# Kernel optimization log

Measured on AMD Instinct MI355X. Metric: run time of the kernel, lower is better.

## Reference

```python
import jax, jax.numpy as jnp
import numpy as np

V, E, H, L, T, B = 6500, 192, 6, 6, 512, 32
HS = E // H  # 32
EPS = 1e-5


def setup_inputs() -> dict:
    key = jax.random.key(0)
    ks = jax.random.split(key, 9)
    s = 0.02
    return {
        "idx": jax.random.randint(ks[0], (B, T), 0, V, dtype=jnp.int32),
        "tok_emb": jax.random.normal(ks[1], (V, E), dtype=jnp.float32) * s,
        "Wq": jax.random.normal(ks[2], (L, E, E), dtype=jnp.float32) * s,
        "Wk": jax.random.normal(ks[3], (L, E, E), dtype=jnp.float32) * s,
        "Wv": jax.random.normal(ks[4], (L, E, E), dtype=jnp.float32) * s,
        "Wo": jax.random.normal(ks[5], (L, E, E), dtype=jnp.float32) * s,
        "W1": jax.random.normal(ks[6], (L, E, 4 * E), dtype=jnp.float32) * s,
        "W2": jax.random.normal(ks[7], (L, 4 * E, E), dtype=jnp.float32) * s,
        "ln1_g": jnp.ones((L, E)), "ln1_b": jnp.zeros((L, E)),
        "ln2_g": jnp.ones((L, E)), "ln2_b": jnp.zeros((L, E)),
        "lnf_g": jnp.ones((E,)), "lnf_b": jnp.zeros((E,)),
        "Wlm": jax.random.normal(ks[8], (E, V), dtype=jnp.float32) * s,
    }


def _layer_norm(x, g, b):
    mu = jnp.mean(x, axis=-1, keepdims=True)
    var = jnp.mean(jnp.square(x - mu), axis=-1, keepdims=True)
    return (x - mu) * jax.lax.rsqrt(var + EPS) * g + b


def _sinusoidal(t, d):
    pos = jnp.arange(t, dtype=jnp.float32)[:, None]
    div = jnp.exp(jnp.arange(0, d, 2, dtype=jnp.float32) * (-np.log(10000.0) / d))
    pe = jnp.zeros((t, d), dtype=jnp.float32)
    pe = pe.at[:, 0::2].set(jnp.sin(pos * div))
    pe = pe.at[:, 1::2].set(jnp.cos(pos * div))
    return pe


def reference(idx, tok_emb, Wq, Wk, Wv, Wo, W1, W2,
              ln1_g, ln1_b, ln2_g, ln2_b, lnf_g, lnf_b, Wlm):
    x = tok_emb[idx] + _sinusoidal(T, E)[None, :, :]  # [B,T,E]
    mask = jnp.tril(jnp.ones((T, T), dtype=bool))
    scale = E ** (-0.5)  # NOTE: original scales by n_embd**-0.5, not head_size

    def block(x, p):
        l1g, l1b, wq, wk, wv, wo, l2g, l2b, w1, w2 = p
        h = _layer_norm(x, l1g, l1b)
        q = jnp.einsum('bte,ehd->bhtd', h, wq.reshape(E, H, HS))
        k = jnp.einsum('bte,ehd->bhtd', h, wk.reshape(E, H, HS))
        v = jnp.einsum('bte,ehd->bhtd', h, wv.reshape(E, H, HS))
        wei = jnp.einsum('bhtd,bhsd->bhts', q, k) * scale  # [B,H,T,T]
        wei = jnp.where(mask, wei, -jnp.inf)
        wei = jax.nn.softmax(wei, axis=-1)
        att = jnp.einsum('bhts,bhsd->bthd', wei, v).reshape(B, T, E)
        x = x + att @ wo
        h2 = _layer_norm(x, l2g, l2b)
        x = x + jax.nn.gelu(h2 @ w1, approximate=False) @ w2
        return x, None

    x, _ = jax.lax.scan(block, x, (ln1_g, ln1_b, Wq, Wk, Wv, Wo, ln2_g, ln2_b, W1, W2))
    x = _layer_norm(x, lnf_g, lnf_b)
    return x @ Wlm  # [B,T,V] logits
```

## Files before the change

### kernel.cpp

```cpp
#include <hip/hip_runtime.h>
#include <hip/hip_bf16.h>
#include <math.h>

#define VOCAB 6500
#define EMB   192
#define NH    6
#define NL    6
#define SEQ   512
#define BATCH 32
#define HSZ   32
#define BT    (BATCH*SEQ)

typedef __attribute__((ext_vector_type(8))) short bh8;
typedef __attribute__((ext_vector_type(4))) float f32x4;

#define ATT_SCALE 0.07216878364870323f

__global__ __launch_bounds__(256) void embed_ln(
    const int* __restrict__ idx, const float* __restrict__ tok,
    const float* __restrict__ g, const float* __restrict__ b,
    float* __restrict__ x, __hip_bfloat16* __restrict__ h) {
  const int wid = threadIdx.x >> 6, lane = threadIdx.x & 63;
  const int bt = blockIdx.x * 4 + wid;
  const int t  = bt & (SEQ - 1);
  const int tokid = idx[bt];
  float v[3];
  #pragma unroll
  for (int i = 0; i < 3; ++i) {
    const int e = lane + i * 64;
    const int i2 = e & ~1;
    const float div = expf((float)i2 * (-9.210340371976184f / (float)EMB));
    const float ang = (float)t * div;
    const float pe  = (e & 1) ? cosf(ang) : sinf(ang);
    v[i] = tok[(size_t)tokid * EMB + e] + pe;
  }
  float s = v[0] + v[1] + v[2];
  #pragma unroll
  for (int o = 32; o; o >>= 1) s += __shfl_xor(s, o);
  const float mu = s * (1.0f / (float)EMB);
  float vs = 0.f;
  #pragma unroll
  for (int i = 0; i < 3; ++i) { const float d = v[i] - mu; vs += d * d; }
  #pragma unroll
  for (int o = 32; o; o >>= 1) vs += __shfl_xor(vs, o);
  const float r = rsqrtf(vs * (1.0f / (float)EMB) + 1e-5f);
  float* xr = x + (size_t)bt * EMB;
  __hip_bfloat16* hr = h + (size_t)bt * EMB;
  #pragma unroll
  for (int i = 0; i < 3; ++i) {
    const int e = lane + i * 64;
    xr[e] = v[i];
    hr[e] = __float2bfloat16((v[i] - mu) * r * g[e] + b[e]);
  }
}

__global__ __launch_bounds__(256) void wprep(
    const float* __restrict__ Wq, const float* __restrict__ Wk,
    const float* __restrict__ Wv, const float* __restrict__ Wo,
    const float* __restrict__ W1, const float* __restrict__ W2,
    const float* __restrict__ Wlm,
    __hip_bfloat16* __restrict__ wqkv, __hip_bfloat16* __restrict__ wot,
    __hip_bfloat16* __restrict__ w1t,  __hip_bfloat16* __restrict__ w2t,
    __hip_bfloat16* __restrict__ wlt) {
  __shared__ float t[32][33];
  const int id = blockIdx.x;
  const float* Ws; __hip_bfloat16* Wd; int K, N, bx, by;
  if (id < 864) {
    const int z = id / 36, rem = id % 36;
    const int sel = z / NL, layer = z % NL;
    by = rem / 6; bx = rem % 6; K = 192; N = 192;
    const float* s4[4] = {Wq, Wk, Wv, Wo};
    Ws = s4[sel] + (size_t)layer * 192 * 192;
    Wd = (sel < 3) ? wqkv + ((size_t)layer * 576 + sel * 192) * 192
                   : wot  + (size_t)layer * 192 * 192;
  } else if (id < 1728) {
    const int j = id - 864, layer = j / 144, rem = j % 144;
    bx = rem % 24; by = rem / 24; K = 192; N = 768;
    Ws = W1 + (size_t)layer * 192 * 768;
    Wd = w1t + (size_t)layer * 768 * 192;
  } else if (id < 2592) {
    const int j = id - 1728, layer = j / 144, rem = j % 144;
    bx = rem % 6; by = rem / 6; K = 768; N = 192;
    Ws = W2 + (size_t)layer * 768 * 192;
    Wd = w2t + (size_t)layer * 192 * 768;
  } else {
    const int j = id - 2592;
    bx = j % 204; by = j / 204; K = 192; N = VOCAB;
    Ws = Wlm; Wd = wlt;
  }
  const int kt = by * 32, nt = bx * 32;
  const int tx = threadIdx.x & 31, ty = threadIdx.x >> 5;
  for (int i = ty; i < 32; i += 8) {
    const int k = kt + i, n = nt + tx;
    t[i][tx] = (k < K && n < N) ? Ws[(size_t)k * N + n] : 0.f;
  }
  __syncthreads();
  for (int i = ty; i < 32; i += 8) {
    const int n = nt + i, k = kt + tx;
    if (n < N && k < K) Wd[(size_t)n * K + k] = __float2bfloat16(t[tx][i]);
  }
}

template<int EPI, int BN>
__global__ __launch_bounds__(256) void gemm_big(
    const __hip_bfloat16* __restrict__ A, const __hip_bfloat16* __restrict__ Bt,
    void* __restrict__ Cv, int M, int N, int K) {
  constexpr int LDK = 72;
  constexpr int NB = BN / 32;
  constexpr int NC = BN / 16;
  __shared__ short As[128 * LDK];
  __shared__ short Bs[BN * LDK];
  const int tid = threadIdx.x;
  const int wid = tid >> 6, lane = tid & 63;
  const int m0 = blockIdx.y * 128, n0 = blockIdx.x * BN;
  const int srow = tid >> 3, schk = tid & 7;
  const int fr = lane & 15, fg = lane >> 4;

  f32x4 acc[2][NC];
  #pragma unroll
  for (int rt = 0; rt < 2; ++rt)
    #pragma unroll
    for (int ct = 0; ct < NC; ++ct) acc[rt][ct] = (f32x4){0.f, 0.f, 0.f, 0.f};

  bh8 av[4], bv[NB];
  #pragma unroll
  for (int p = 0; p < 4; ++p)
    av[p] = *reinterpret_cast<const bh8*>(A + (size_t)(m0 + srow + p * 32) * K + schk * 8);
  #pragma unroll
  for (int p = 0; p < NB; ++p) {
    const int nr = n0 + srow + p * 32;
    if (nr < N) bv[p] = *reinterpret_cast<const bh8*>(Bt + (size_t)nr * K + schk * 8);
    else        bv[p] = (bh8){0,0,0,0,0,0,0,0};
  }

  for (int k0 = 0; k0 < K; k0 += 64) {
    __syncthreads();
    #pragma unroll
    for (int p = 0; p < 4; ++p)
      *reinterpret_cast<bh8*>(As + (srow + p * 32) * LDK + schk * 8) = av[p];
    #pragma unroll
    for (int p = 0; p < NB; ++p)
      *reinterpret_cast<bh8*>(Bs + (srow + p * 32) * LDK + schk * 8) = bv[p];
    __syncthreads();
    if (k0 + 64 < K) {
      const int kn = k0 + 64 + schk * 8;
      #pragma unroll
      for (int p = 0; p < 4; ++p)
        av[p] = *reinterpret_cast<const bh8*>(A + (size_t)(m0 + srow + p * 32) * K + kn);
      #pragma unroll
      for (int p = 0; p < NB; ++p) {
        const int nr = n0 + srow + p * 32;
        if (nr < N) bv[p] = *reinterpret_cast<const bh8*>(Bt + (size_t)nr * K + kn);
      }
    }
    #pragma unroll
    for (int s = 0; s < 2; ++s) {
      bh8 af[2];
      #pragma unroll
      for (int rt = 0; rt < 2; ++rt)
        af[rt] = *reinterpret_cast<const bh8*>(As + (wid * 32 + rt * 16 + fr) * LDK + s * 32 + fg * 8);
      #pragma unroll
      for (int ct = 0; ct < NC; ++ct) {
        const bh8 bf_ = *reinterpret_cast<const bh8*>(Bs + (ct * 16 + fr) * LDK + s * 32 + fg * 8);
        #pragma unroll
        for (int rt = 0; rt < 2; ++rt)
          acc[rt][ct] = __builtin_amdgcn_mfma_f32_16x16x32_bf16(af[rt], bf_, acc[rt][ct], 0, 0, 0);
      }
    }
  }

  #pragma unroll
  for (int rt = 0; rt < 2; ++rt)
    #pragma unroll
    for (int ct = 0; ct < NC; ++ct) {
      const int col = n0 + ct * 16 + fr;
      if (col < N) {
        #pragma unroll
        for (int rr = 0; rr < 4; ++rr) {
          const int row = m0 + wid * 32 + rt * 16 + fg * 4 + rr;
          float v = acc[rt][ct][rr];
          if (EPI == 0) {
            ((float*)Cv)[(size_t)row * N + col] = v;
          } else if (EPI == 2) {
            v = 0.5f * v * (1.0f + erff(v * 0.70710678118654752f));
            ((__hip_bfloat16*)Cv)[(size_t)row * N + col] = __float2bfloat16(v);
          } else {
            const int part = col / 192, c2 = col - part * 192;
            if (part == 0) v *= ATT_SCALE;
            const int bb = row >> 9, tt = row & (SEQ - 1);
            const int hh = c2 >> 5, dd = c2 & (HSZ - 1);
            ((__hip_bfloat16*)Cv)[(size_t)part * BT * EMB +
                (((size_t)(bb * NH + hh)) * SEQ + tt) * HSZ + dd] = __float2bfloat16(v);
          }
        }
      }
    }
}

__global__ __launch_bounds__(128) void gemm_resln(
    const __hip_bfloat16* __restrict__ A, const __hip_bfloat16* __restrict__ Bt,
    float* __restrict__ X, __hip_bfloat16* __restrict__ Hout,
    const float* __restrict__ g, const float* __restrict__ b, int K) {
  constexpr int LDK = 72;
  __shared__ short As[32 * LDK];
  __shared__ short Bs[192 * LDK];
  const int tid = threadIdx.x;
  const int wid = tid >> 6, lane = tid & 63;
  const int m0 = blockIdx.x * 32;
  const int srow = tid >> 3, schk = tid & 7;
  const int fr = lane & 15, fg = lane >> 4;

  f32x4 acc[12];
  #pragma unroll
  for (int j = 0; j < 12; ++j) acc[j] = (f32x4){0.f, 0.f, 0.f, 0.f};

  bh8 av[2], bv[12];
  #pragma unroll
  for (int p = 0; p < 2; ++p)
    av[p] = *reinterpret_cast<const bh8*>(A + (size_t)(m0 + srow + p * 16) * K + schk * 8);
  #pragma unroll
  for (int p = 0; p < 12; ++p)
    bv[p] = *reinterpret_cast<const bh8*>(Bt + (size_t)(srow + p * 16) * K + schk * 8);

  for (int k0 = 0; k0 < K; k0 += 64) {
    __syncthreads();
    #pragma unroll
    for (int p = 0; p < 2; ++p)
      *reinterpret_cast<bh8*>(As + (srow + p * 16) * LDK + schk * 8) = av[p];
    #pragma unroll
    for (int p = 0; p < 12; ++p)
      *reinterpret_cast<bh8*>(Bs + (srow + p * 16) * LDK + schk * 8) = bv[p];
    __syncthreads();
    if (k0 + 64 < K) {
      const int kn = k0 + 64 + schk * 8;
      #pragma unroll
      for (int p = 0; p < 2; ++p)
        av[p] = *reinterpret_cast<const bh8*>(A + (size_t)(m0 + srow + p * 16) * K + kn);
      #pragma unroll
      for (int p = 0; p < 12; ++p)
        bv[p] = *reinterpret_cast<const bh8*>(Bt + (size_t)(srow + p * 16) * K + kn);
    }
    #pragma unroll
    for (int s = 0; s < 2; ++s) {
      const bh8 af = *reinterpret_cast<const bh8*>(As + (wid * 16 + fr) * LDK + s * 32 + fg * 8);
      #pragma unroll
      for (int j = 0; j < 12; ++j) {
        const bh8 bf_ = *reinterpret_cast<const bh8*>(Bs + (j * 16 + fr) * LDK + s * 32 + fg * 8);
        acc[j] = __builtin_amdgcn_mfma_f32_16x16x32_bf16(af, bf_, acc[j], 0, 0, 0);
      }
    }
  }

  #pragma unroll
  for (int rr = 0; rr < 4; ++rr) {
    const int row = m0 + wid * 16 + fg * 4 + rr;
    float v[12], sum = 0.f, sq = 0.f;
    #pragma unroll
    for (int j = 0; j < 12; ++j) {
      v[j] = acc[j][rr] + X[(size_t)row * EMB + j * 16 + fr];
      sum += v[j]; sq += v[j] * v[j];
    }
    #pragma unroll
    for (int o = 8; o; o >>= 1) {
      sum += __shfl_xor(sum, o);
      sq  += __shfl_xor(sq,  o);
    }
    const float mu = sum * (1.0f / (float)EMB);
    const float r  = rsqrtf(sq * (1.0f / (float)EMB) - mu * mu + 1e-5f);
    #pragma unroll
    for (int j = 0; j < 12; ++j) {
      const int col = j * 16 + fr;
      X[(size_t)row * EMB + col] = v[j];
      Hout[(size_t)row * EMB + col] = __float2bfloat16((v[j] - mu) * r * g[col] + b[col]);
    }
  }
}

__global__ __launch_bounds__(256) void flash_attn(
    const __hip_bfloat16* __restrict__ qh, const __hip_bfloat16* __restrict__ kh,
    const __hip_bfloat16* __restrict__ vh, __hip_bfloat16* __restrict__ att) {
  constexpr int QT = 128, KT = 128;
  constexpr int LK = 40;
  constexpr int LS = 136;
  __shared__ __hip_bfloat16 Ks[KT * LK];
  __shared__ __hip_bfloat16 Vs[HSZ * LS];
  __shared__ __hip_bfloat16 Ps[4][32 * LS];
  const int qt = (SEQ / QT - 1) - blockIdx.x;
  const int h = blockIdx.y, b = blockIdx.z;
  const int tid = threadIdx.x, wid = tid >> 6, lane = tid & 63;
  const int q0 = qt * QT;
  const size_t hb = ((size_t)(b * NH + h)) * SEQ * HSZ;
  const int fr = lane & 15, fg = lane >> 4;

  bh8 aq[2];
  #pragma unroll
  for (int rt = 0; rt < 2; ++rt)
    aq[rt] = *reinterpret_cast<const bh8*>(
        qh + hb + (size_t)(q0 + wid * 32 + rt * 16 + fr) * HSZ + fg * 8);

  f32x4 o[2][2];
  float lp[2][4];
  #pragma unroll
  for (int rt = 0; rt < 2; ++rt) {
    #pragma unroll
    for (int ct = 0; ct < 2; ++ct) o[rt][ct] = (f32x4){0.f, 0.f, 0.f, 0.f};
    #pragma unroll
    for (int rr = 0; rr < 4; ++rr) lp[rt][rr] = 0.f;
  }

  const int nt = qt + 1;
  const int sr = tid >> 1;
  const int dbase = (tid & 1) * 16;
  bh8 kv[2], vv[2];
  #pragma unroll
  for (int i = 0; i < 2; ++i) {
    kv[i] = *reinterpret_cast<const bh8*>(kh + hb + (size_t)sr * HSZ + dbase + i * 8);
    vv[i] = *reinterpret_cast<const bh8*>(vh + hb + (size_t)sr * HSZ + dbase + i * 8);
  }

  for (int it = 0; it < nt; ++it) {
    const int s0 = it * KT;
    __syncthreads();
    #pragma unroll
    for (int i = 0; i < 2; ++i) {
      const int d0 = dbase + i * 8;
      *reinterpret_cast<bh8*>(&Ks[sr * LK + d0]) = kv[i];
      short tmp[8]; *reinterpret_cast<bh8*>(tmp) = vv[i];
      #pragma unroll
      for (int j = 0; j < 8; ++j)
        Vs[(d0 + j) * LS + sr] = *reinterpret_cast<__hip_bfloat16*>(&tmp[j]);
    }
    __syncthreads();
    if (it + 1 < nt) {
      const size_t nb_ = hb + (size_t)(s0 + KT + sr) * HSZ + dbase;
      #pragma unroll
      for (int i = 0; i < 2; ++i) {
        kv[i] = *reinterpret_cast<const bh8*>(kh + nb_ + i * 8);
        vv[i] = *reinterpret_cast<const bh8*>(vh + nb_ + i * 8);
      }
    }

    f32x4 sfr[2][8];
    #pragma unroll
    for (int rt = 0; rt < 2; ++rt)
      #pragma unroll
      for (int st = 0; st < 8; ++st) {
        const bh8 bf_ = *reinterpret_cast<const bh8*>(&Ks[(st * 16 + fr) * LK + fg * 8]);
        sfr[rt][st] = __builtin_amdgcn_mfma_f32_16x16x32_bf16(
            aq[rt], bf_, (f32x4){0.f, 0.f, 0.f, 0.f}, 0, 0, 0);
      }

    __hip_bfloat16* Pw = Ps[wid];
    const bool diag = (s0 + KT - 1 > q0 + wid * 32);
    #pragma unroll
    for (int rt = 0; rt < 2; ++rt) {
      #pragma unroll
      for (int rr = 0; rr < 4; ++rr) {
        float pr[8];
        if (diag) {
          const int qa = q0 + wid * 32 + rt * 16 + fg * 4 + rr;
          #pragma unroll
          for (int st = 0; st < 8; ++st) {
            const int sa = s0 + st * 16 + fr;
            pr[st] = (sa > qa) ? 0.f : __expf(sfr[rt][st][rr]);
          }
        } else {
          #pragma unroll
          for (int st = 0; st < 8; ++st) pr[st] = __expf(sfr[rt][st][rr]);
        }
        float ls = 0.f;
        #pragma unroll
        for (int st = 0; st < 8; ++st) ls += pr[st];
        lp[rt][rr] += ls;
        #pragma unroll
        for (int st = 0; st < 8; ++st)
          Pw[(rt * 16 + fg * 4 + rr) * LS + st * 16 + fr] = __float2bfloat16(pr[st]);
      }
    }

    #pragma unroll
    for (int ks = 0; ks < 4; ++ks) {
      bh8 vb_[2];
      #pragma unroll
      for (int ct = 0; ct < 2; ++ct)
        vb_[ct] = *reinterpret_cast<const bh8*>(&Vs[(ct * 16 + fr) * LS + ks * 32 + fg * 8]);
      #pragma unroll
      for (int rt = 0; rt < 2; ++rt) {
        const bh8 pa = *reinterpret_cast<const bh8*>(&Pw[(rt * 16 + fr) * LS + ks * 32 + fg * 8]);
        #pragma unroll
        for (int ct = 0; ct < 2; ++ct)
          o[rt][ct] = __builtin_amdgcn_mfma_f32_16x16x32_bf16(pa, vb_[ct], o[rt][ct], 0, 0, 0);
      }
    }
  }

  #pragma unroll
  for (int rt = 0; rt < 2; ++rt)
    #pragma unroll
    for (int rr = 0; rr < 4; ++rr) {
      float s = lp[rt][rr];
      #pragma unroll
      for (int off = 8; off; off >>= 1) s += __shfl_xor(s, off);
      const float inv = 1.0f / s;
      const int qa = q0 + wid * 32 + rt * 16 + fg * 4 + rr;
      #pragma unroll
      for (int ct = 0; ct < 2; ++ct) {
        const int d = ct * 16 + fr;
        att[((size_t)(b * SEQ + qa)) * EMB + h * HSZ + d] =
            __float2bfloat16(o[rt][ct][rr] * inv);
      }
    }
}

extern "C" void kernel_launch(void* const* d_in, const int* in_sizes, int n_in,
                              void* d_out, int out_size, void* d_ws, size_t ws_size,
                              hipStream_t stream) {
  const int*   idx   = (const int*)  d_in[0];
  const float* tok   = (const float*)d_in[1];
  const float* Wq    = (const float*)d_in[2];
  const float* Wk    = (const float*)d_in[3];
  const float* Wv    = (const float*)d_in[4];
  const float* Wo    = (const float*)d_in[5];
  const float* W1    = (const float*)d_in[6];
  const float* W2    = (const float*)d_in[7];
  const float* ln1g  = (const float*)d_in[8];
  const float* ln1b  = (const float*)d_in[9];
  const float* ln2g  = (const float*)d_in[10];
  const float* ln2b  = (const float*)d_in[11];
  const float* lnfg  = (const float*)d_in[12];
  const float* lnfb  = (const float*)d_in[13];
  const float* Wlm   = (const float*)d_in[14];
  float* out = (float*)d_out;

  const size_t NTE = (size_t)BT * EMB;
  char* ws = (char*)d_ws;
  float* x   = (float*)ws;                         ws += NTE * 4;
  __hip_bfloat16* qh   = (__hip_bfloat16*)ws;      ws += NTE * 2 * 3;
  __hip_bfloat16* h    = (__hip_bfloat16*)ws;      ws += NTE * 2;
  __hip_bfloat16* att  = (__hip_bfloat16*)ws;      ws += NTE * 2;
  __hip_bfloat16* hid  = (__hip_bfloat16*)ws;      ws += NTE * 4 * 2;
  __hip_bfloat16* wqkv = (__hip_bfloat16*)ws;      ws += (size_t)NL * 576 * EMB * 2;
  __hip_bfloat16* wot  = (__hip_bfloat16*)ws;      ws += (size_t)NL * EMB * EMB * 2;
  __hip_bfloat16* w1t  = (__hip_bfloat16*)ws;      ws += (size_t)NL * EMB * EMB * 4 * 2;
  __hip_bfloat16* w2t  = (__hip_bfloat16*)ws;      ws += (size_t)NL * EMB * EMB * 4 * 2;
  __hip_bfloat16* wlt  = (__hip_bfloat16*)ws;

  wprep<<<3816, 256, 0, stream>>>(Wq, Wk, Wv, Wo, W1, W2, Wlm,
                                  wqkv, wot, w1t, w2t, wlt);
  embed_ln<<<BT / 4, 256, 0, stream>>>(idx, tok, ln1g, ln1b, x, h);

  const dim3 gQKV(576 / 64, BT / 128);
  const dim3 gM  (EMB * 4 / 64, BT / 128);
  const dim3 gV  ((VOCAB + 127) / 128, BT / 128);
  const dim3 gA  (SEQ / 128, NH, BATCH);

  for (int l = 0; l < NL; ++l) {
    const size_t wo = (size_t)l * EMB * EMB;
    const size_t wm = (size_t)l * EMB * EMB * 4;
    gemm_big<3, 64><<<gQKV, 256, 0, stream>>>(h, wqkv + (size_t)l * 576 * EMB, qh, BT, 576, EMB);
    flash_attn<<<gA, 256, 0, stream>>>(qh, qh + NTE, qh + 2 * NTE, att);
    gemm_resln<<<BT / 32, 128, 0, stream>>>(att, wot + wo, x, h,
                                            ln2g + l * EMB, ln2b + l * EMB, EMB);
    gemm_big<2, 64><<<gM, 256, 0, stream>>>(h, w1t + wm, hid, BT, EMB * 4, EMB);
    const float* ng = (l == NL - 1) ? lnfg : ln1g + (l + 1) * EMB;
    const float* nb = (l == NL - 1) ? lnfb : ln1b + (l + 1) * EMB;
    gemm_resln<<<BT / 32, 128, 0, stream>>>(hid, w2t + wm, x, h, ng, nb, EMB * 4);
  }

  gemm_big<0, 128><<<gV, 256, 0, stream>>>(h, wlt, out, BT, VOCAB, EMB);
}
```

Measured before the change: 704.8 us.

## Fuse residual-LayerNorm GEMMs with following W1/QKV projections via LDS-staged activations

Adds a resln_fused kernel that computes the residual projection GEMM plus LayerNorm, keeps the normalized 32-row tile in LDS, and immediately multiplies it by the next layer's W1 (with GELU) or the next QKV weight. The separate QKV and W1 GEMM launches and the round trip of the normalized activations through global memory are removed. Attention softmax now uses exp2f, with log2(e) folded into the Q scale. The fused second GEMM runs on only 32 rows per 128-thread block and streams its weights from global memory without LDS reuse, so it may be less efficient than the larger-tiled gemm_big.

```diff
diff --git a/kernel.cpp b/kernel.cpp
--- a/kernel.cpp
+++ b/kernel.cpp
@@ -14,44 +14,11 @@
 typedef __attribute__((ext_vector_type(8))) short bh8;
 typedef __attribute__((ext_vector_type(4))) float f32x4;
 
-#define ATT_SCALE 0.07216878364870323f
-
-__global__ __launch_bounds__(256) void embed_ln(
-    const int* __restrict__ idx, const float* __restrict__ tok,
-    const float* __restrict__ g, const float* __restrict__ b,
-    float* __restrict__ x, __hip_bfloat16* __restrict__ h) {
-  const int wid = threadIdx.x >> 6, lane = threadIdx.x & 63;
-  const int bt = blockIdx.x * 4 + wid;
-  const int t  = bt & (SEQ - 1);
-  const int tokid = idx[bt];
-  float v[3];
-  #pragma unroll
-  for (int i = 0; i < 3; ++i) {
-    const int e = lane + i * 64;
-    const int i2 = e & ~1;
-    const float div = expf((float)i2 * (-9.210340371976184f / (float)EMB));
-    const float ang = (float)t * div;
-    const float pe  = (e & 1) ? cosf(ang) : sinf(ang);
-    v[i] = tok[(size_t)tokid * EMB + e] + pe;
-  }
-  float s = v[0] + v[1] + v[2];
-  #pragma unroll
-  for (int o = 32; o; o >>= 1) s += __shfl_xor(s, o);
-  const float mu = s * (1.0f / (float)EMB);
-  float vs = 0.f;
-  #pragma unroll
-  for (int i = 0; i < 3; ++i) { const float d = v[i] - mu; vs += d * d; }
-  #pragma unroll
-  for (int o = 32; o; o >>= 1) vs += __shfl_xor(vs, o);
-  const float r = rsqrtf(vs * (1.0f / (float)EMB) + 1e-5f);
-  float* xr = x + (size_t)bt * EMB;
-  __hip_bfloat16* hr = h + (size_t)bt * EMB;
-  #pragma unroll
-  for (int i = 0; i < 3; ++i) {
-    const int e = lane + i * 64;
-    xr[e] = v[i];
-    hr[e] = __float2bfloat16((v[i] - mu) * r * g[e] + b[e]);
-  }
+#define ATT_SCALE_L2E 0.10413996713994119f
+
+static __device__ __forceinline__ short bf16s(float v) {
+  __hip_bfloat16 t = __float2bfloat16(v);
+  return *reinterpret_cast<short*>(&t);
 }
 
 __global__ __launch_bounds__(256) void wprep(
@@ -101,6 +68,42 @@
   }
 }
 
+__global__ __launch_bounds__(256) void embed_ln(
+    const int* __restrict__ idx, const float* __restrict__ tok,
+    const float* __restrict__ g, const float* __restrict__ b,
+    float* __restrict__ x, __hip_bfloat16* __restrict__ h) {
+  const int wid = threadIdx.x >> 6, lane = threadIdx.x & 63;
+  const int bt = blockIdx.x * 4 + wid;
+  const int t  = bt & (SEQ - 1);
+  const int tokid = idx[bt];
+  float v[3];
+  #pragma unroll
+  for (int i = 0; i < 3; ++i) {
+    const int e = lane + i * 64;
+    const int i2 = e & ~1;
+    const float div = expf((float)i2 * (-9.210340371976184f / (float)EMB));
+    const float ang = (float)t * div;
+    const float pe  = (e & 1) ? cosf(ang) : sinf(ang);
+    v[i] = tok[(size_t)tokid * EMB + e] + pe;
+  }
+  float s = v[0] + v[1] + v[2];
+  #pragma unroll
+  for (int o = 32; o; o >>= 1) s += __shfl_xor(s, o);
+  const float mu = s * (1.0f / (float)EMB);
+  float vs = 0.f;
+  #pragma unroll
+  for (int i = 0; i < 3; ++i) { const float d = v[i] - mu; vs += d * d; }
+  #pragma unroll
+  for (int o = 32; o; o >>= 1) vs += __shfl_xor(vs, o);
+  const float r = rsqrtf(vs * (1.0f / (float)EMB) + 1e-5f);
+  #pragma unroll
+  for (int i = 0; i < 3; ++i) {
+    const int e = lane + i * 64;
+    x[(size_t)bt * EMB + e] = v[i];
+    h[(size_t)bt * EMB + e] = __float2bfloat16((v[i] - mu) * r * g[e] + b[e]);
+  }
+}
+
 template<int EPI, int BN>
 __global__ __launch_bounds__(256) void gemm_big(
     const __hip_bfloat16* __restrict__ A, const __hip_bfloat16* __restrict__ Bt,
@@ -181,12 +184,9 @@
           float v = acc[rt][ct][rr];
           if (EPI == 0) {
             ((float*)Cv)[(size_t)row * N + col] = v;
-          } else if (EPI == 2) {
-            v = 0.5f * v * (1.0f + erff(v * 0.70710678118654752f));
-            ((__hip_bfloat16*)Cv)[(size_t)row * N + col] = __float2bfloat16(v);
           } else {
             const int part = col / 192, c2 = col - part * 192;
-            if (part == 0) v *= ATT_SCALE;
+            if (part == 0) v *= ATT_SCALE_L2E;
             const int bb = row >> 9, tt = row & (SEQ - 1);
             const int hh = c2 >> 5, dd = c2 & (HSZ - 1);
             ((__hip_bfloat16*)Cv)[(size_t)part * BT * EMB +
@@ -272,6 +272,145 @@
       const int col = j * 16 + fr;
       X[(size_t)row * EMB + col] = v[j];
       Hout[(size_t)row * EMB + col] = __float2bfloat16((v[j] - mu) * r * g[col] + b[col]);
+    }
+  }
+}
+
+template<int P2>
+__global__ __launch_bounds__(128) void resln_fused(
+    const __hip_bfloat16* __restrict__ A, const __hip_bfloat16* __restrict__ B1t,
+    float* __restrict__ X, const float* __restrict__ g, const float* __restrict__ b,
+    int K1, const __hip_bfloat16* __restrict__ B2t,
+    __hip_bfloat16* __restrict__ Out2) {
+  constexpr int N2 = (P2 == 1) ? 768 : 576;
+  constexpr int NT = N2 / 16;
+  constexpr int LDK = 72;
+  constexpr int LDH = 200;
+  __shared__ short As[32 * LDK];
+  __shared__ short Bs[192 * LDK];
+  __shared__ short Hs[32 * LDH];
+  const int tid = threadIdx.x;
+  const int wid = tid >> 6, lane = tid & 63;
+  const int m0 = blockIdx.x * 32;
+  const int srow = tid >> 3, schk = tid & 7;
+  const int fr = lane & 15, fg = lane >> 4;
+
+  f32x4 acc[12];
+  #pragma unroll
+  for (int j = 0; j < 12; ++j) acc[j] = (f32x4){0.f, 0.f, 0.f, 0.f};
+
+  bh8 av[2], bv[12];
+  #pragma unroll
+  for (int p = 0; p < 2; ++p)
+    av[p] = *reinterpret_cast<const bh8*>(A + (size_t)(m0 + srow + p * 16) * K1 + schk * 8);
+  #pragma unroll
+  for (int p = 0; p < 12; ++p)
+    bv[p] = *reinterpret_cast<const bh8*>(B1t + (size_t)(srow + p * 16) * K1 + schk * 8);
+
+  for (int k0 = 0; k0 < K1; k0 += 64) {
+    __syncthreads();
+    #pragma unroll
+    for (int p = 0; p < 2; ++p)
+      *reinterpret_cast<bh8*>(As + (srow + p * 16) * LDK + schk * 8) = av[p];
+    #pragma unroll
+    for (int p = 0; p < 12; ++p)
+      *reinterpret_cast<bh8*>(Bs + (srow + p * 16) * LDK + schk * 8) = bv[p];
+    __syncthreads();
+    if (k0 + 64 < K1) {
+      const int kn = k0 + 64 + schk * 8;
+      #pragma unroll
+      for (int p = 0; p < 2; ++p)
+        av[p] = *reinterpret_cast<const bh8*>(A + (size_t)(m0 + srow + p * 16) * K1 + kn);
+      #pragma unroll
+      for (int p = 0; p < 12; ++p)
+        bv[p] = *reinterpret_cast<const bh8*>(B1t + (size_t)(srow + p * 16) * K1 + kn);
+    }
+    #pragma unroll
+    for (int s = 0; s < 2; ++s) {
+      const bh8 af = *reinterpret_cast<const bh8*>(As + (wid * 16 + fr) * LDK + s * 32 + fg * 8);
+      #pragma unroll
+      for (int j = 0; j < 12; ++j) {
+        const bh8 bf_ = *reinterpret_cast<const bh8*>(Bs + (j * 16 + fr) * LDK + s * 32 + fg * 8);
+        acc[j] = __builtin_amdgcn_mfma_f32_16x16x32_bf16(af, bf_, acc[j], 0, 0, 0);
+      }
+    }
+  }
+
+  #pragma unroll
+  for (int rr = 0; rr < 4; ++rr) {
+    const int lrow = wid * 16 + fg * 4 + rr;
+    const int row = m0 + lrow;
+    float v[12], sum = 0.f, sq = 0.f;
+    #pragma unroll
+    for (int j = 0; j < 12; ++j) {
+      v[j] = acc[j][rr] + X[(size_t)row * EMB + j * 16 + fr];
+      sum += v[j]; sq += v[j] * v[j];
+    }
+    #pragma unroll
+    for (int o = 8; o; o >>= 1) {
+      sum += __shfl_xor(sum, o);
+      sq  += __shfl_xor(sq,  o);
+    }
+    const float mu = sum * (1.0f / (float)EMB);
+    const float r  = rsqrtf(sq * (1.0f / (float)EMB) - mu * mu + 1e-5f);
+    #pragma unroll
+    for (int j = 0; j < 12; ++j) {
+      const int col = j * 16 + fr;
+      X[(size_t)row * EMB + col] = v[j];
+      Hs[lrow * LDH + col] = bf16s((v[j] - mu) * r * g[col] + b[col]);
+    }
+  }
+  __syncthreads();
+
+  bh8 af2[2][6];
+  #pragma unroll
+  for (int mt = 0; mt < 2; ++mt)
+    #pragma unroll
+    for (int kk = 0; kk < 6; ++kk)
+      af2[mt][kk] = *reinterpret_cast<const bh8*>(Hs + (mt * 16 + fr) * LDH + kk * 32 + fg * 8);
+
+  bh8 bcur[6], bnxt[6];
+  #pragma unroll
+  for (int kk = 0; kk < 6; ++kk)
+    bcur[kk] = *reinterpret_cast<const bh8*>(B2t + (size_t)(wid * 16 + fr) * 192 + kk * 32 + fg * 8);
+
+  for (int ntile = wid; ntile < NT; ntile += 2) {
+    const int nnext = ntile + 2;
+    if (nnext < NT) {
+      #pragma unroll
+      for (int kk = 0; kk < 6; ++kk)
+        bnxt[kk] = *reinterpret_cast<const bh8*>(B2t + (size_t)(nnext * 16 + fr) * 192 + kk * 32 + fg * 8);
+    }
+    f32x4 a2[2];
+    a2[0] = (f32x4){0.f, 0.f, 0.f, 0.f};
+    a2[1] = (f32x4){0.f, 0.f, 0.f, 0.f};
+    #pragma unroll
+    for (int kk = 0; kk < 6; ++kk) {
+      a2[0] = __builtin_amdgcn_mfma_f32_16x16x32_bf16(af2[0][kk], bcur[kk], a2[0], 0, 0, 0);
+      a2[1] = __builtin_amdgcn_mfma_f32_16x16x32_bf16(af2[1][kk], bcur[kk], a2[1], 0, 0, 0);
+    }
+    const int col = ntile * 16 + fr;
+    #pragma unroll
+    for (int mt = 0; mt < 2; ++mt)
+      #pragma unroll
+      for (int rr = 0; rr < 4; ++rr) {
+        const int row = m0 + mt * 16 + fg * 4 + rr;
+        float v = a2[mt][rr];
+        if (P2 == 1) {
+          v = 0.5f * v * (1.0f + erff(v * 0.70710678118654752f));
+          Out2[(size_t)row * 768 + col] = __float2bfloat16(v);
+        } else {
+          const int part = col / 192, c2 = col - part * 192;
+          if (part == 0) v *= ATT_SCALE_L2E;
+          const int bb = row >> 9, tt = row & (SEQ - 1);
+          const int hh = c2 >> 5, dd = c2 & (HSZ - 1);
+          Out2[(size_t)part * BT * EMB +
+               (((size_t)(bb * NH + hh)) * SEQ + tt) * HSZ + dd] = __float2bfloat16(v);
+        }
+      }
+    if (nnext < NT) {
+      #pragma unroll
+      for (int kk = 0; kk < 6; ++kk) bcur[kk] = bnxt[kk];
     }
   }
 }
@@ -362,11 +501,11 @@
           #pragma unroll
           for (int st = 0; st < 8; ++st) {
             const int sa = s0 + st * 16 + fr;
-            pr[st] = (sa > qa) ? 0.f : __expf(sfr[rt][st][rr]);
+            pr[st] = (sa > qa) ? 0.f : exp2f(sfr[rt][st][rr]);
           }
         } else {
           #pragma unroll
-          for (int st = 0; st < 8; ++st) pr[st] = __expf(sfr[rt][st][rr]);
+          for (int st = 0; st < 8; ++st) pr[st] = exp2f(sfr[rt][st][rr]);
         }
         float ls = 0.f;
         #pragma unroll
@@ -450,21 +589,24 @@
   embed_ln<<<BT / 4, 256, 0, stream>>>(idx, tok, ln1g, ln1b, x, h);
 
   const dim3 gQKV(576 / 64, BT / 128);
-  const dim3 gM  (EMB * 4 / 64, BT / 128);
   const dim3 gV  ((VOCAB + 127) / 128, BT / 128);
   const dim3 gA  (SEQ / 128, NH, BATCH);
+
+  gemm_big<3, 64><<<gQKV, 256, 0, stream>>>(h, wqkv, qh, BT, 576, EMB);
 
   for (int l = 0; l < NL; ++l) {
     const size_t wo = (size_t)l * EMB * EMB;
     const size_t wm = (size_t)l * EMB * EMB * 4;
-    gemm_big<3, 64><<<gQKV, 256, 0, stream>>>(h, wqkv + (size_t)l * 576 * EMB, qh, BT, 576, EMB);
     flash_attn<<<gA, 256, 0, stream>>>(qh, qh + NTE, qh + 2 * NTE, att);
-    gemm_resln<<<BT / 32, 128, 0, stream>>>(att, wot + wo, x, h,
-                                            ln2g + l * EMB, ln2b + l * EMB, EMB);
-    gemm_big<2, 64><<<gM, 256, 0, stream>>>(h, w1t + wm, hid, BT, EMB * 4, EMB);
-    const float* ng = (l == NL - 1) ? lnfg : ln1g + (l + 1) * EMB;
-    const float* nb = (l == NL - 1) ? lnfb : ln1b + (l + 1) * EMB;
-    gemm_resln<<<BT / 32, 128, 0, stream>>>(hid, w2t + wm, x, h, ng, nb, EMB * 4);
+    resln_fused<1><<<BT / 32, 128, 0, stream>>>(
+        att, wot + wo, x, ln2g + l * EMB, ln2b + l * EMB, EMB, w1t + wm, hid);
+    if (l < NL - 1) {
+      resln_fused<2><<<BT / 32, 128, 0, stream>>>(
+          hid, w2t + wm, x, ln1g + (l + 1) * EMB, ln1b + (l + 1) * EMB, EMB * 4,
+          wqkv + (size_t)(l + 1) * 576 * EMB, qh);
+    } else {
+      gemm_resln<<<BT / 32, 128, 0, stream>>>(hid, w2t + wm, x, h, lnfg, lnfb, EMB * 4);
+    }
   }
 
   gemm_big<0, 128><<<gV, 256, 0, stream>>>(h, wlt, out, BT, VOCAB, EMB);
```

New measurement: 778.6 us. +10.5%, slower.
